# Kernel tuning notes

Hardware: AMD Instinct MI355X
Metric: run time of the kernel (lower is better)

## Reference

```python
import jax, jax.numpy as jnp
import numpy as np
import math

FRAME_SIZE = 576
GAMMA = 0.5
NUM_HEADS = 32


def rotate_half(x):
    x1, x2 = jnp.split(x, 2, axis=-1)
    return jnp.concatenate([-x2, x1], axis=-1)


def apply_rope(x, freqs):
    return x * jnp.cos(freqs) + rotate_half(x) * jnp.sin(freqs)


def rope_freqs(length, dim):
    theta = 10000.0 ** (-jnp.arange(0, dim, 2, dtype=jnp.float32) / dim)
    f = jnp.arange(length, dtype=jnp.float32)[:, None] * theta[None, :]  # [L, dim/2]
    return jnp.concatenate([f, f], axis=-1)  # [L, dim]


def setup_inputs() -> dict:
    key = jax.random.key(0)
    ks = jax.random.split(key, 9)
    B, T, C = 2, 2048, 2048
    s = 0.02  # init scale for projection weights
    return {
        "hidden_states": jax.random.normal(ks[0], (B, T, C), jnp.float32),
        "Wq": jax.random.normal(ks[1], (C, C), jnp.float32) * s,
        "bq": jnp.zeros((C,), jnp.float32),
        "Wk": jax.random.normal(ks[2], (C, C), jnp.float32) * s,
        "bk": jnp.zeros((C,), jnp.float32),
        "Wv": jax.random.normal(ks[3], (C, C), jnp.float32) * s,
        "bv": jnp.zeros((C,), jnp.float32),
        "Wo": jax.random.normal(ks[4], (C, C), jnp.float32) * s,
        "bo": jnp.zeros((C,), jnp.float32),
    }


def reference(hidden_states, Wq, bq, Wk, bk, Wv, bv, Wo, bo):
    B, T, C = hidden_states.shape
    H = NUM_HEADS
    dh = C // H

    def split_heads(x):
        return x.reshape(B, T, H, dh).transpose(0, 2, 1, 3)  # [B,H,T,dh]

    q = split_heads(hidden_states @ Wq.T + bq)
    k = split_heads(hidden_states @ Wk.T + bk)
    v = split_heads(hidden_states @ Wv.T + bv)

    # Dual RoPE: absolute positions, then temporal (frame-level) positions.
    freqs_abs = rope_freqs(T, dh)[None, None]  # [1,1,T,dh]
    q = apply_rope(q, freqs_abs)
    k = apply_rope(k, freqs_abs)

    temporal_ids = jnp.floor((jnp.arange(T) // FRAME_SIZE).astype(jnp.float32) * GAMMA).astype(jnp.int32)
    n_temp = int(math.floor(((T - 1) // FRAME_SIZE) * GAMMA)) + 1
    freqs_temp = rope_freqs(n_temp, dh)[temporal_ids][None, None]  # [1,1,T,dh]
    q = apply_rope(q, freqs_temp)
    k = apply_rope(k, freqs_temp)

    scores = jnp.einsum('bhqd,bhkd->bhqk', q, k) / math.sqrt(dh)
    # build_fwbc_mask reduces to a plain causal mask (inner-loop var leak: j==i).
    causal = jnp.tril(jnp.ones((T, T), dtype=bool))
    scores = jnp.where(causal[None, None], scores, -jnp.inf)
    weights = jax.nn.softmax(scores, axis=-1)

    out = jnp.einsum('bhqk,bhkd->bhqd', weights, v)
    out = out.transpose(0, 2, 1, 3).reshape(B, T, H * dh)
    return out @ Wo.T + bo
```

## Files before the change

kernel.cpp:

```cpp
#include <hip/hip_runtime.h>

#define AS1 __attribute__((address_space(1)))
#define AS3 __attribute__((address_space(3)))

typedef __attribute__((ext_vector_type(8))) short bf16x8;
typedef __attribute__((ext_vector_type(4))) float f32x4;

__device__ __forceinline__ unsigned short f2bf(float f) {
    unsigned int u = __float_as_uint(f);
    u += 0x7fffu + ((u >> 16) & 1u);
    return (unsigned short)(u >> 16);
}
__device__ __forceinline__ float bf2f(unsigned short h) {
    return __uint_as_float(((unsigned int)h) << 16);
}

__device__ __forceinline__ void gload16(const void* g, void* l) {
    __builtin_amdgcn_global_load_lds((const AS1 unsigned int*)g, (AS3 unsigned int*)l, 16, 0, 0);
}

#define MFMA(a, b, c) __builtin_amdgcn_mfma_f32_16x16x32_bf16(a, b, c, 0, 0, 0)

__global__ void cvt_f32_bf16(const float* __restrict__ src, unsigned short* __restrict__ dst, int n4) {
    const int i = blockIdx.x * blockDim.x + threadIdx.x;
    if (i >= n4) return;
    const float4 v = reinterpret_cast<const float4*>(src)[i];
    ushort4 o;
    o.x = f2bf(v.x); o.y = f2bf(v.y); o.z = f2bf(v.z); o.w = f2bf(v.w);
    reinterpret_cast<ushort4*>(dst)[i] = o;
}

__global__ void rope_table(float* __restrict__ cosT, float* __restrict__ sinT) {
    const int i = blockIdx.x * 256 + threadIdx.x;
    const int t = i >> 5, j = i & 31;
    const int fid = t / 576;
    const float p = (float)(t + (fid >> 1));
    const float theta = powf(10000.0f, -(float)j / 32.0f);
    const float ang = p * theta;
    cosT[i] = cosf(ang);
    sinT[i] = sinf(ang);
}

template <int MODE>
__global__ __launch_bounds__(256, 2)
void gemm128(const unsigned short* __restrict__ A,
             const unsigned short* __restrict__ W,
             const float* __restrict__ b0, const float* __restrict__ b1, const float* __restrict__ b2,
             const float* __restrict__ cosT, const float* __restrict__ sinT,
             unsigned short* __restrict__ O0, unsigned short* __restrict__ O1, unsigned short* __restrict__ O2,
             float* __restrict__ Of) {
    constexpr int K = 2048, LDA = 2048;
    const int tid = threadIdx.x;
    const int lane = tid & 63;
    const int w = tid >> 6;
    const int wr = w >> 1, wc = w & 1;
    const int brow = blockIdx.y * 128;
    const int bcol = blockIdx.x * 128;
    const int z = blockIdx.z;
    const unsigned short* Bmat = W + (size_t)z * 4194304;
    const float* bias = (MODE == 1) ? b0 : (z == 0 ? b0 : (z == 1 ? b1 : b2));

    __shared__ unsigned char lds[32768];
    unsigned char* Asm_ = lds;
    unsigned char* Bsm  = lds + 16384;

    f32x4 acc[4][4] = {};
    const int l15 = lane & 15;
    const int lg = lane >> 4;

    for (int kt = 0; kt < K / 64; ++kt) {
        const int k0g = kt * 64;
        __syncthreads();
#pragma unroll
        for (int s = 0; s < 4; ++s) {
            const int c = w * 256 + s * 64 + lane;
            const int row = c >> 3;
            const int cb = (c & 7) ^ (row & 7);
            gload16(A    + (size_t)(brow + row) * LDA + k0g + cb * 8, Asm_ + (w * 256 + s * 64) * 16);
            gload16(Bmat + (size_t)(bcol + row) * LDA + k0g + cb * 8, Bsm  + (w * 256 + s * 64) * 16);
        }
        asm volatile("s_waitcnt vmcnt(0)" ::: "memory");
        __syncthreads();

#pragma unroll
        for (int kk = 0; kk < 2; ++kk) {
            bf16x8 af[4], bfr[4];
            const int koff = kk * 64 + lg * 16;
#pragma unroll
            for (int m = 0; m < 4; ++m) {
                const int row = wr * 64 + m * 16 + l15;
                af[m] = *(const bf16x8*)(Asm_ + row * 128 + (koff ^ ((row & 7) << 4)));
            }
#pragma unroll
            for (int n = 0; n < 4; ++n) {
                const int row = wc * 64 + n * 16 + l15;
                bfr[n] = *(const bf16x8*)(Bsm + row * 128 + (koff ^ ((row & 7) << 4)));
            }
#pragma unroll
            for (int m = 0; m < 4; ++m)
#pragma unroll
                for (int n = 0; n < 4; ++n)
                    acc[m][n] = MFMA(af[m], bfr[n], acc[m][n]);
        }
    }

    if (MODE == 0 && z != 2) {
        unsigned short* Ot = (z == 0 ? O0 : O1);
#pragma unroll
        for (int m = 0; m < 4; ++m) {
#pragma unroll
            for (int n2 = 0; n2 < 2; ++n2) {
                const int d1 = n2 * 16 + l15;
                const int cg1 = bcol + wc * 64 + d1;
                const float bv1 = bias[cg1], bv2 = bias[cg1 + 32];
                const int hh = cg1 >> 6;
#pragma unroll
                for (int r = 0; r < 4; ++r) {
                    const int rg = brow + wr * 64 + m * 16 + lg * 4 + r;
                    const int bb = rg >> 11, t = rg & 2047;
                    const float v1 = acc[m][n2][r] + bv1;
                    const float v2 = acc[m][n2 + 2][r] + bv2;
                    const float c = cosT[t * 32 + d1];
                    const float s = sinT[t * 32 + d1];
                    unsigned short* base = Ot + (((size_t)bb * 32 + hh) * 2048 + t) * 64;
                    base[d1]      = f2bf(v1 * c - v2 * s);
                    base[d1 + 32] = f2bf(v2 * c + v1 * s);
                }
            }
        }
    } else {
#pragma unroll
        for (int m = 0; m < 4; ++m) {
#pragma unroll
            for (int n = 0; n < 4; ++n) {
                const int cg = bcol + wc * 64 + n * 16 + l15;
                const float bv_ = bias[cg];
#pragma unroll
                for (int r = 0; r < 4; ++r) {
                    const int rg = brow + wr * 64 + m * 16 + lg * 4 + r;
                    const float v = acc[m][n][r] + bv_;
                    if (MODE == 0) {
                        const int bb = rg >> 11, t = rg & 2047, hh = cg >> 6, d = cg & 63;
                        O2[(((size_t)bb * 32 + hh) * 64 + d) * 2048 + t] = f2bf(v);
                    } else {
                        Of[(size_t)rg * 2048 + cg] = v;
                    }
                }
            }
        }
    }
}

__global__ __launch_bounds__(256, 4)
void attn(const unsigned short* __restrict__ Qg, const unsigned short* __restrict__ Kg,
          const unsigned short* __restrict__ Vtg, unsigned short* __restrict__ Og) {
    const int d0 = blockIdx.x;
    const int xcd = d0 & 7, ii = d0 >> 3;
    const int bh = xcd * 8 + (ii >> 4);
    const int pp = ii & 15;
    const int b = bh >> 5, h = bh & 31;
    const int tid = threadIdx.x;
    const int lane = tid & 63;
    const int w = tid >> 6;
    const int l15 = lane & 15, lg = lane >> 4;

    const unsigned short* Q  = Qg  + (size_t)bh * 131072;
    const unsigned short* K  = Kg  + (size_t)bh * 131072;
    const unsigned short* Vt = Vtg + (size_t)bh * 131072;

    __shared__ unsigned char Ks[2][8192];
    __shared__ unsigned char Vs[2][8192];
    __shared__ unsigned char Ps[4][2048];

    const int cA = (w << 6) + lane, cB = cA + 256;
    const int rA = cA >> 3, bA_ = (cA & 7) ^ (rA & 7);
    const int rB = cB >> 3, bB_ = (cB & 7) ^ (rB & 7);
    const int dstA = (w << 10);
    const int dstB = 4096 + (w << 10);

#define STAGE(kt_, buf_)                                                          \
    do {                                                                          \
        const int ko = (kt_) * 64;                                                \
        gload16(K  + (size_t)(ko + rA) * 64 + bA_ * 8, Ks[buf_] + dstA);          \
        gload16(K  + (size_t)(ko + rB) * 64 + bB_ * 8, Ks[buf_] + dstB);          \
        gload16(Vt + (size_t)rA * 2048 + ko + bA_ * 8, Vs[buf_] + dstA);          \
        gload16(Vt + (size_t)rB * 2048 + ko + bB_ * 8, Vs[buf_] + dstB);          \
    } while (0)

    constexpr float SCALE = 0.125f * 1.4426950408889634f;

    for (int pass = 0; pass < 2; ++pass) {
        const int qt = pass ? (31 - pp) : pp;
        const int qbase = qt * 64 + w * 16;

        bf16x8 qf[2];
#pragma unroll
        for (int h2 = 0; h2 < 2; ++h2)
            qf[h2] = *(const bf16x8*)(Q + (size_t)(qbase + l15) * 64 + h2 * 32 + lg * 8);

        f32x4 oacc[4] = {};
        float mrow[4], lrow[4];
#pragma unroll
        for (int r = 0; r < 4; ++r) { mrow[r] = -1e30f; lrow[r] = 0.f; }

        __syncthreads();
        const int ntiles = qt + 1;
        STAGE(0, 0);

        for (int kt = 0; kt < ntiles; ++kt) {
            const int buf = kt & 1;
            asm volatile("s_waitcnt vmcnt(0)" ::: "memory");
            __syncthreads();
            if (kt + 1 < ntiles) STAGE(kt + 1, buf ^ 1);

            const bool diag = (kt == qt);
            const int ntmax = diag ? w : 3;

            f32x4 sac[4];
#pragma unroll
            for (int nt = 0; nt < 4; ++nt) {
                sac[nt] = f32x4{0.f, 0.f, 0.f, 0.f};
                if (nt <= ntmax) {
#pragma unroll
                    for (int h2 = 0; h2 < 2; ++h2) {
                        const int kcol = nt * 16 + l15;
                        const int koff = h2 * 64 + lg * 16;
                        const bf16x8 kf = *(const bf16x8*)(Ks[buf] + kcol * 128 + (koff ^ ((kcol & 7) << 4)));
                        sac[nt] = MFMA(qf[h2], kf, sac[nt]);
                    }
                }
            }

            float pmax[4] = {-1e30f, -1e30f, -1e30f, -1e30f};
#pragma unroll
            for (int nt = 0; nt < 4; ++nt) {
                if (nt <= ntmax) {
#pragma unroll
                    for (int r = 0; r < 4; ++r) {
                        float sv = sac[nt][r] * SCALE;
                        if (diag && nt == w && (l15 > lg * 4 + r)) sv = -1e30f;
                        sac[nt][r] = sv;
                        pmax[r] = fmaxf(pmax[r], sv);
                    }
                }
            }
#pragma unroll
            for (int mk = 1; mk < 16; mk <<= 1)
#pragma unroll
                for (int r = 0; r < 4; ++r)
                    pmax[r] = fmaxf(pmax[r], __shfl_xor(pmax[r], mk));

            const float dm = fmaxf(fmaxf(pmax[0] - mrow[0], pmax[1] - mrow[1]),
                                   fmaxf(pmax[2] - mrow[2], pmax[3] - mrow[3]));
            if (!__all(dm <= 8.0f)) {
#pragma unroll
                for (int r = 0; r < 4; ++r) {
                    const float mnew = fmaxf(mrow[r], pmax[r]);
                    const float sc = exp2f(mrow[r] - mnew);
                    mrow[r] = mnew;
                    lrow[r] *= sc;
#pragma unroll
                    for (int dt = 0; dt < 4; ++dt) oacc[dt][r] *= sc;
                }
            }

            float ps[4] = {0.f, 0.f, 0.f, 0.f};
#pragma unroll
            for (int nt = 0; nt < 4; ++nt) {
#pragma unroll
                for (int r = 0; r < 4; ++r) {
                    float pv = 0.f;
                    if (nt <= ntmax) { pv = exp2f(sac[nt][r] - mrow[r]); ps[r] += pv; }
                    const int qrow = lg * 4 + r;
                    const int kcol = nt * 16 + l15;
                    *(unsigned short*)(Ps[w] + qrow * 128 + ((kcol * 2) ^ ((qrow & 7) << 4))) = f2bf(pv);
                }
            }
#pragma unroll
            for (int r = 0; r < 4; ++r) lrow[r] += ps[r];

            asm volatile("s_waitcnt lgkmcnt(0)" ::: "memory");
            __builtin_amdgcn_sched_barrier(0);

            const int h2max = (ntmax >= 2) ? 1 : 0;
#pragma unroll
            for (int h2 = 0; h2 < 2; ++h2) {
                if (h2 > h2max) continue;
                const int koff = h2 * 64 + lg * 16;
                const bf16x8 pf = *(const bf16x8*)(Ps[w] + l15 * 128 + (koff ^ ((l15 & 7) << 4)));
#pragma unroll
                for (int dt = 0; dt < 4; ++dt) {
                    const int dcol = dt * 16 + l15;
                    const bf16x8 vf = *(const bf16x8*)(Vs[buf] + dcol * 128 + (koff ^ ((dcol & 7) << 4)));
                    oacc[dt] = MFMA(pf, vf, oacc[dt]);
                }
            }
        }

        float lr[4];
#pragma unroll
        for (int r = 0; r < 4; ++r) {
            float t = lrow[r];
#pragma unroll
            for (int mk = 1; mk < 16; mk <<= 1) t += __shfl_xor(t, mk);
            lr[r] = t;
        }
#pragma unroll
        for (int dt = 0; dt < 4; ++dt) {
#pragma unroll
            for (int r = 0; r < 4; ++r) {
                const int t = qbase + lg * 4 + r;
                const float v = oacc[dt][r] / lr[r];
                Og[(size_t)(b * 2048 + t) * 2048 + h * 64 + dt * 16 + l15] = f2bf(v);
            }
        }
    }
#undef STAGE
}

extern "C" void kernel_launch(void* const* d_in, const int* in_sizes, int n_in,
                              void* d_out, int out_size, void* d_ws, size_t ws_size,
                              hipStream_t stream) {
    const float* hs = (const float*)d_in[0];
    const float* Wq = (const float*)d_in[1];
    const float* bq = (const float*)d_in[2];
    const float* Wk = (const float*)d_in[3];
    const float* bk = (const float*)d_in[4];
    const float* Wv = (const float*)d_in[5];
    const float* bv = (const float*)d_in[6];
    const float* Wo = (const float*)d_in[7];
    const float* bo = (const float*)d_in[8];
    float* out = (float*)d_out;

    char* ws = (char*)d_ws;
    unsigned short* Xb = (unsigned short*)ws;
    unsigned short* Wb = (unsigned short*)(ws + (16u << 20));
    unsigned short* Qb = (unsigned short*)(ws + (48u << 20));
    unsigned short* Kb = (unsigned short*)(ws + (64u << 20));
    unsigned short* Vtb = (unsigned short*)(ws + (80u << 20));
    unsigned short* Ob = Xb;
    float* cosT = (float*)(ws + (96u << 20));
    float* sinT = cosT + 65536;

    cvt_f32_bf16<<<8192, 256, 0, stream>>>(hs, Xb, 2097152);
    cvt_f32_bf16<<<4096, 256, 0, stream>>>(Wq, Wb + (size_t)0 * 4194304, 1048576);
    cvt_f32_bf16<<<4096, 256, 0, stream>>>(Wk, Wb + (size_t)1 * 4194304, 1048576);
    cvt_f32_bf16<<<4096, 256, 0, stream>>>(Wv, Wb + (size_t)2 * 4194304, 1048576);
    cvt_f32_bf16<<<4096, 256, 0, stream>>>(Wo, Wb + (size_t)3 * 4194304, 1048576);
    rope_table<<<256, 256, 0, stream>>>(cosT, sinT);

    gemm128<0><<<dim3(16, 32, 3), 256, 0, stream>>>(Xb, Wb, bq, bk, bv, cosT, sinT, Qb, Kb, Vtb, nullptr);

    attn<<<dim3(1024), 256, 0, stream>>>(Qb, Kb, Vtb, Ob);

    gemm128<1><<<dim3(16, 32, 1), 256, 0, stream>>>(Ob, Wb + (size_t)3 * 4194304, bo, bo, bo,
                                                    cosT, sinT, nullptr, nullptr, nullptr, out);
}
```

Measured before the change: 300.1 us.

## Transpose S=K·Q^T in attention, fold softmax scale into Q, pack P stores

Computes the score tile as K·Qᵀ so each lane holds one query row. The row max and sum then need only two cross-lane shuffles instead of four per row times four rows. The softmax scale and log2e factor are folded into the Q projection epilogue, which removes the per-score multiply. P is packed into 64-bit bf16 stores instead of scalar 16-bit writes, and setprio hints wrap the MFMA sections. The cost is an extra shuffle to redistribute the rescale factors to the output layout, plus a change in where Q is rounded to bf16.

```diff
diff --git a/kernel.cpp b/kernel.cpp
--- a/kernel.cpp
+++ b/kernel.cpp
@@ -1,4 +1,5 @@
 #include <hip/hip_runtime.h>
+#include <hip/hip_bf16.h>
 
 #define AS1 __attribute__((address_space(1)))
 #define AS3 __attribute__((address_space(3)))
@@ -11,8 +12,10 @@
     u += 0x7fffu + ((u >> 16) & 1u);
     return (unsigned short)(u >> 16);
 }
-__device__ __forceinline__ float bf2f(unsigned short h) {
-    return __uint_as_float(((unsigned int)h) << 16);
+
+__device__ __forceinline__ unsigned int pk2bf(float a, float b) {
+    __hip_bfloat162 h = __float22bfloat162_rn(make_float2(a, b));
+    return *reinterpret_cast<unsigned int*>(&h);
 }
 
 __device__ __forceinline__ void gload16(const void* g, void* l) {
@@ -105,6 +108,7 @@
     }
 
     if (MODE == 0 && z != 2) {
+        const float qsc = (z == 0) ? 0.18033688011112042f : 1.0f;
         unsigned short* Ot = (z == 0 ? O0 : O1);
 #pragma unroll
         for (int m = 0; m < 4; ++m) {
@@ -123,8 +127,8 @@
                     const float c = cosT[t * 32 + d1];
                     const float s = sinT[t * 32 + d1];
                     unsigned short* base = Ot + (((size_t)bb * 32 + hh) * 2048 + t) * 64;
-                    base[d1]      = f2bf(v1 * c - v2 * s);
-                    base[d1 + 32] = f2bf(v2 * c + v1 * s);
+                    base[d1]      = f2bf((v1 * c - v2 * s) * qsc);
+                    base[d1 + 32] = f2bf((v2 * c + v1 * s) * qsc);
                 }
             }
         }
@@ -187,7 +191,9 @@
         gload16(Vt + (size_t)rB * 2048 + ko + bB_ * 8, Vs[buf_] + dstB);          \
     } while (0)
 
-    constexpr float SCALE = 0.125f * 1.4426950408889634f;
+    const int pbase = l15 * 128;
+    const int pswz = (l15 & 7) << 4;
+    const int lg8 = lg * 8;
 
     for (int pass = 0; pass < 2; ++pass) {
         const int qt = pass ? (31 - pp) : pp;
@@ -199,9 +205,8 @@
             qf[h2] = *(const bf16x8*)(Q + (size_t)(qbase + l15) * 64 + h2 * 32 + lg * 8);
 
         f32x4 oacc[4] = {};
-        float mrow[4], lrow[4];
-#pragma unroll
-        for (int r = 0; r < 4; ++r) { mrow[r] = -1e30f; lrow[r] = 0.f; }
+        float m = -1e30f;
+        float l = 0.f;
 
         __syncthreads();
         const int ntiles = qt + 1;
@@ -216,78 +221,82 @@
             const bool diag = (kt == qt);
             const int ntmax = diag ? w : 3;
 
-            f32x4 sac[4];
+            f32x4 sac[4] = {};
+            __builtin_amdgcn_s_setprio(1);
 #pragma unroll
             for (int nt = 0; nt < 4; ++nt) {
-                sac[nt] = f32x4{0.f, 0.f, 0.f, 0.f};
                 if (nt <= ntmax) {
 #pragma unroll
                     for (int h2 = 0; h2 < 2; ++h2) {
                         const int kcol = nt * 16 + l15;
                         const int koff = h2 * 64 + lg * 16;
                         const bf16x8 kf = *(const bf16x8*)(Ks[buf] + kcol * 128 + (koff ^ ((kcol & 7) << 4)));
-                        sac[nt] = MFMA(qf[h2], kf, sac[nt]);
+                        sac[nt] = MFMA(kf, qf[h2], sac[nt]);
                     }
                 }
             }
-
-            float pmax[4] = {-1e30f, -1e30f, -1e30f, -1e30f};
+            __builtin_amdgcn_s_setprio(0);
+
+            if (diag) {
+#pragma unroll
+                for (int nt = 0; nt < 4; ++nt) {
+                    if (nt == w) {
+#pragma unroll
+                        for (int r = 0; r < 4; ++r)
+                            if (lg * 4 + r > l15) sac[nt][r] = -1e30f;
+                    }
+                }
+            }
+
+            float pm = -1e30f;
 #pragma unroll
             for (int nt = 0; nt < 4; ++nt) {
                 if (nt <= ntmax) {
 #pragma unroll
-                    for (int r = 0; r < 4; ++r) {
-                        float sv = sac[nt][r] * SCALE;
-                        if (diag && nt == w && (l15 > lg * 4 + r)) sv = -1e30f;
-                        sac[nt][r] = sv;
-                        pmax[r] = fmaxf(pmax[r], sv);
-                    }
-                }
-            }
-#pragma unroll
-            for (int mk = 1; mk < 16; mk <<= 1)
-#pragma unroll
-                for (int r = 0; r < 4; ++r)
-                    pmax[r] = fmaxf(pmax[r], __shfl_xor(pmax[r], mk));
-
-            const float dm = fmaxf(fmaxf(pmax[0] - mrow[0], pmax[1] - mrow[1]),
-                                   fmaxf(pmax[2] - mrow[2], pmax[3] - mrow[3]));
-            if (!__all(dm <= 8.0f)) {
-#pragma unroll
-                for (int r = 0; r < 4; ++r) {
-                    const float mnew = fmaxf(mrow[r], pmax[r]);
-                    const float sc = exp2f(mrow[r] - mnew);
-                    mrow[r] = mnew;
-                    lrow[r] *= sc;
-#pragma unroll
-                    for (int dt = 0; dt < 4; ++dt) oacc[dt][r] *= sc;
-                }
-            }
-
-            float ps[4] = {0.f, 0.f, 0.f, 0.f};
+                    for (int r = 0; r < 4; ++r) pm = fmaxf(pm, sac[nt][r]);
+                }
+            }
+            pm = fmaxf(pm, __shfl_xor(pm, 16));
+            pm = fmaxf(pm, __shfl_xor(pm, 32));
+
+            if (!__all(pm - m <= 8.0f)) {
+                const float mn = fmaxf(m, pm);
+                const float sc = exp2f(m - mn);
+                m = mn;
+                l *= sc;
+                float scp[4];
+#pragma unroll
+                for (int r = 0; r < 4; ++r) scp[r] = __shfl(sc, (lg << 2) + r);
+#pragma unroll
+                for (int dt = 0; dt < 4; ++dt)
+#pragma unroll
+                    for (int r = 0; r < 4; ++r) oacc[dt][r] *= scp[r];
+            }
+
 #pragma unroll
             for (int nt = 0; nt < 4; ++nt) {
-#pragma unroll
-                for (int r = 0; r < 4; ++r) {
-                    float pv = 0.f;
-                    if (nt <= ntmax) { pv = exp2f(sac[nt][r] - mrow[r]); ps[r] += pv; }
-                    const int qrow = lg * 4 + r;
-                    const int kcol = nt * 16 + l15;
-                    *(unsigned short*)(Ps[w] + qrow * 128 + ((kcol * 2) ^ ((qrow & 7) << 4))) = f2bf(pv);
-                }
-            }
-#pragma unroll
-            for (int r = 0; r < 4; ++r) lrow[r] += ps[r];
+                unsigned long long pk = 0;
+                if (nt <= ntmax) {
+                    const float p0 = exp2f(sac[nt][0] - m);
+                    const float p1 = exp2f(sac[nt][1] - m);
+                    const float p2 = exp2f(sac[nt][2] - m);
+                    const float p3 = exp2f(sac[nt][3] - m);
+                    l += (p0 + p1) + (p2 + p3);
+                    pk = ((unsigned long long)pk2bf(p2, p3) << 32) | pk2bf(p0, p1);
+                }
+                *(unsigned long long*)(Ps[w] + pbase + ((nt * 32 + lg8) ^ pswz)) = pk;
+            }
 
             asm volatile("s_waitcnt lgkmcnt(0)" ::: "memory");
             __builtin_amdgcn_sched_barrier(0);
 
             const int h2max = (ntmax >= 2) ? 1 : 0;
+            __builtin_amdgcn_s_setprio(1);
 #pragma unroll
             for (int h2 = 0; h2 < 2; ++h2) {
                 if (h2 > h2max) continue;
                 const int koff = h2 * 64 + lg * 16;
-                const bf16x8 pf = *(const bf16x8*)(Ps[w] + l15 * 128 + (koff ^ ((l15 & 7) << 4)));
+                const bf16x8 pf = *(const bf16x8*)(Ps[w] + pbase + (koff ^ pswz));
 #pragma unroll
                 for (int dt = 0; dt < 4; ++dt) {
                     const int dcol = dt * 16 + l15;
@@ -295,22 +304,21 @@
                     oacc[dt] = MFMA(pf, vf, oacc[dt]);
                 }
             }
-        }
-
-        float lr[4];
-#pragma unroll
-        for (int r = 0; r < 4; ++r) {
-            float t = lrow[r];
-#pragma unroll
-            for (int mk = 1; mk < 16; mk <<= 1) t += __shfl_xor(t, mk);
-            lr[r] = t;
-        }
+            __builtin_amdgcn_s_setprio(0);
+        }
+
+        float lf = l;
+        lf += __shfl_xor(lf, 16);
+        lf += __shfl_xor(lf, 32);
+        float lq[4];
+#pragma unroll
+        for (int r = 0; r < 4; ++r) lq[r] = __shfl(lf, (lg << 2) + r);
 #pragma unroll
         for (int dt = 0; dt < 4; ++dt) {
 #pragma unroll
             for (int r = 0; r < 4; ++r) {
                 const int t = qbase + lg * 4 + r;
-                const float v = oacc[dt][r] / lr[r];
+                const float v = oacc[dt][r] / lq[r];
                 Og[(size_t)(b * 2048 + t) * 2048 + h * 64 + dt * 16 + l15] = f2bf(v);
             }
         }
```

Measured after the change: 273.9 us. 8.7% less time.
